# Kernel optimization log

Hardware: AMD Instinct MI355X
Metric: run time of the kernel (lower is better)

## Reference

```python
import jax, jax.numpy as jnp
import numpy as np

H, DH, HID = 8, 16, 128
N_USER, N_ITEM, N_TASTE, N_IMAGE = 20000, 50000, 50000, 50000


def setup_inputs() -> dict:
    key = jax.random.key(0)
    ks = jax.random.split(key, 24)
    f = jax.random.normal
    s = 1.0 / np.sqrt(HID).astype(np.float32)
    inp = {
        "x_user": f(ks[0], (N_USER, HID), jnp.float32),
        "x_item": f(ks[1], (N_ITEM, HID), jnp.float32),
        "x_taste": f(ks[2], (N_TASTE, HID), jnp.float32),
        "x_image": f(ks[3], (N_IMAGE, HID), jnp.float32),
        "Wk": f(ks[4], (4, HID, HID), jnp.float32) * s,
        "bk": jnp.zeros((4, HID), jnp.float32),
        "Wq": f(ks[5], (4, HID, HID), jnp.float32) * s,
        "bq": jnp.zeros((4, HID), jnp.float32),
        "Wv": f(ks[6], (4, HID, HID), jnp.float32) * s,
        "bv": jnp.zeros((4, HID), jnp.float32),
        "a_rel": f(ks[7], (4, H, DH, DH), jnp.float32) * (1.0 / np.sqrt(DH).astype(np.float32)),
        "m_rel": f(ks[8], (4, H, DH, DH), jnp.float32) * (1.0 / np.sqrt(DH).astype(np.float32)),
        "p_rel": jnp.ones((4, H), jnp.float32),
        "Wo": f(ks[9], (2, HID, HID), jnp.float32) * s,
        "bo": jnp.zeros((2, HID), jnp.float32),
        "skip": jnp.ones((2,), jnp.float32),
        "ti_src": jax.random.randint(ks[10], (50000,), 0, N_TASTE, jnp.int32),
        "ti_dst": jax.random.randint(ks[11], (50000,), 0, N_ITEM, jnp.int32),
        "im_src": jax.random.randint(ks[12], (50000,), 0, N_IMAGE, jnp.int32),
        "im_dst": jax.random.randint(ks[13], (50000,), 0, N_ITEM, jnp.int32),
        "ub_src": jax.random.randint(ks[14], (500000,), 0, N_USER, jnp.int32),
        "ub_dst": jax.random.randint(ks[15], (500000,), 0, N_ITEM, jnp.int32),
        "bu_src": jax.random.randint(ks[16], (500000,), 0, N_ITEM, jnp.int32),
        "bu_dst": jax.random.randint(ks[17], (500000,), 0, N_USER, jnp.int32),
    }
    return inp


def _kqv(x, i, Wk, bk, Wq, bq, Wv, bv):
    k = (x @ Wk[i] + bk[i]).reshape(-1, H, DH)
    q = (x @ Wq[i] + bq[i]).reshape(-1, H, DH)
    v = (x @ Wv[i] + bv[i]).reshape(-1, H, DH)
    return k, q, v


def _edge_alpha_msg(k_src, v_src, q_dst, src, dst, a, m, p):
    # per-edge-type relation transform at node level, then gather per edge
    kr = jnp.einsum('nhd,hde->nhe', k_src, a)  # [Nsrc,H,DH]
    vr = jnp.einsum('nhd,hde->nhe', v_src, m)
    alpha = (q_dst[dst] * kr[src]).sum(-1) * p * (1.0 / np.sqrt(DH).astype(np.float32))  # [E,H]
    return alpha, vr[src]


def _seg_softmax_agg(alpha, msg, dst, n):
    amax = jax.ops.segment_max(alpha, dst, num_segments=n)
    amax = jnp.where(jnp.isfinite(amax), amax, 0.0)
    ex = jnp.exp(alpha - amax[dst])
    den = jax.ops.segment_sum(ex, dst, num_segments=n)
    w = ex / (den[dst] + 1e-16)
    return jax.ops.segment_sum(msg * w[..., None], dst, num_segments=n)  # [n,H,DH]


def reference(x_user, x_item, x_taste, x_image, Wk, bk, Wq, bq, Wv, bv,
              a_rel, m_rel, p_rel, Wo, bo, skip,
              ti_src, ti_dst, im_src, im_dst, ub_src, ub_dst, bu_src, bu_dst):
    k_u, q_u, v_u = _kqv(x_user, 0, Wk, bk, Wq, bq, Wv, bv)
    k_i, q_i, v_i = _kqv(x_item, 1, Wk, bk, Wq, bq, Wv, bv)
    k_t, _, v_t = _kqv(x_taste, 2, Wk, bk, Wq, bq, Wv, bv)
    k_g, _, v_g = _kqv(x_image, 3, Wk, bk, Wq, bq, Wv, bv)

    # edges into 'item': taste(0), image(1), user-buys(2); softmax over all combined per item
    a0, m0 = _edge_alpha_msg(k_t, v_t, q_i, ti_src, ti_dst, a_rel[0], m_rel[0], p_rel[0])
    a1, m1 = _edge_alpha_msg(k_g, v_g, q_i, im_src, im_dst, a_rel[1], m_rel[1], p_rel[1])
    a2, m2 = _edge_alpha_msg(k_u, v_u, q_i, ub_src, ub_dst, a_rel[2], m_rel[2], p_rel[2])
    alpha_i = jnp.concatenate([a0, a1, a2], 0)
    msg_i = jnp.concatenate([m0, m1, m2], 0)
    dst_i = jnp.concatenate([ti_dst, im_dst, ub_dst], 0)
    agg_i = _seg_softmax_agg(alpha_i, msg_i, dst_i, N_ITEM)

    # edges into 'user': item-bought_by(3)
    a3, m3 = _edge_alpha_msg(k_i, v_i, q_u, bu_src, bu_dst, a_rel[3], m_rel[3], p_rel[3])
    agg_u = _seg_softmax_agg(a3, m3, bu_dst, N_USER)

    out_i = jax.nn.gelu(agg_i.reshape(-1, HID), approximate=False) @ Wo[0] + bo[0]
    g_i = jax.nn.sigmoid(skip[0])
    out_i = g_i * out_i + (1.0 - g_i) * x_item

    out_u = jax.nn.gelu(agg_u.reshape(-1, HID), approximate=False) @ Wo[1] + bo[1]
    g_u = jax.nn.sigmoid(skip[1])
    out_u = g_u * out_u + (1.0 - g_u) * x_user
    return (out_i, out_u)
```

## Files before the change

kernel.cpp:

```cpp
#include <hip/hip_runtime.h>
#include <math.h>


namespace {
constexpr int HIDN  = 128;
constexpr int NHEAD = 8;

constexpr int NU = 20000, NI = 50000, NT = 50000, NG = 50000;
constexpr int E_TI = 50000, E_IM = 50000, E_UB = 500000, E_BU = 500000;
constexpr int ETOT = E_TI + E_IM + E_UB + E_BU;
constexpr int ND   = NI + NU;

constexpr int BASE_U = 0;
constexpr int BASE_I = NU;
constexpr int BASE_T = NU + NI;
constexpr int BASE_G = NU + NI + NT;

constexpr int NMAT = 12;
constexpr int MATSZ = 128 * 128;
constexpr int SU = 136;

constexpr int NBU = (NU + 63) / 64;
constexpr int NBI = (NI + 63) / 64;
constexpr int NBT = (NT + 63) / 64;
constexpr int NBG = (NG + 63) / 64;
}

typedef __attribute__((ext_vector_type(8))) short short8v;
typedef __attribute__((ext_vector_type(4))) float f32x4;
typedef __attribute__((ext_vector_type(4))) unsigned short ushort4v;

__device__ __forceinline__ unsigned short bf16rne(float f) {
    unsigned u = __float_as_uint(f);
    unsigned r = (u + 0x7fffu + ((u >> 16) & 1u)) >> 16;
    return (unsigned short)r;
}
__device__ __forceinline__ float bf16f(unsigned short h) {
    return __uint_as_float(((unsigned)h) << 16);
}
__device__ __forceinline__ float bflo(unsigned int u) { return __uint_as_float(u << 16); }
__device__ __forceinline__ float bfhi(unsigned int u) { return __uint_as_float(u & 0xffff0000u); }

__global__ void build_cw_kernel(const float* __restrict__ Wk, const float* __restrict__ bk,
                                const float* __restrict__ Wv, const float* __restrict__ bv,
                                const float* __restrict__ a_rel, const float* __restrict__ m_rel,
                                float* __restrict__ cw)
{
    const int total = 2 * 4 * 129 * 128;
    int idx = blockIdx.x * blockDim.x + threadIdx.x;
    if (idx >= total) return;
    int c     = idx & 127;
    int r     = (idx >> 7) % 129;
    int t     = ((idx >> 7) / 129) & 3;
    int which = idx / (4 * 129 * 128);
    const int et_map[4] = {2, 3, 0, 1};
    int et = et_map[t];
    const float* W = (which == 0 ? Wk : Wv) + (size_t)t * HIDN * HIDN;
    const float* b = (which == 0 ? bk : bv) + (size_t)t * HIDN;
    const float* A = (which == 0 ? a_rel : m_rel) + (size_t)et * NHEAD * 16 * 16;
    int h = c >> 4, e2 = c & 15;
    float s = 0.f;
#pragma unroll
    for (int d = 0; d < 16; ++d) {
        float w = (r == 128) ? b[h * 16 + d] : W[(size_t)r * HIDN + h * 16 + d];
        s = fmaf(w, A[h * 256 + d * 16 + e2], s);
    }
    cw[idx] = s;
}

__global__ void pack_kernel(const float* __restrict__ cw,
                            const float* __restrict__ Wq, const float* __restrict__ bq,
                            const float* __restrict__ Wo, const float* __restrict__ bo,
                            short* __restrict__ pkh, short* __restrict__ pkl,
                            float* __restrict__ bias)
{
    const int total = NMAT * MATSZ + NMAT * HIDN;
    int idx = blockIdx.x * blockDim.x + threadIdx.x;
    if (idx >= total) return;
    if (idx < NMAT * MATSZ) {
        int mat = idx >> 14;
        int rem = idx & (MATSZ - 1);
        int i    = rem & 7;
        int lane = (rem >> 3) & 63;
        int ct   = (rem >> 9) & 7;
        int ks   = rem >> 12;
        int k   = ks * 32 + ((lane >> 4) & 3) * 8 + i;
        int col = ct * 16 + (lane & 15);
        float v;
        if (mat < 8)       v = cw[(size_t)mat * 129 * 128 + (size_t)k * 128 + col];
        else if (mat < 10) v = Wq[(size_t)(mat - 8) * MATSZ + (size_t)k * 128 + col];
        else               v = Wo[(size_t)(mat - 10) * MATSZ + (size_t)k * 128 + col];
        unsigned short hb = bf16rne(v);
        float rest = v - bf16f(hb);
        pkh[idx] = (short)hb;
        pkl[idx] = (short)bf16rne(rest);
    } else {
        int b = idx - NMAT * MATSZ;
        int mat = b >> 7, col = b & 127;
        float v;
        if (mat < 8)       v = cw[(size_t)mat * 129 * 128 + (size_t)128 * 128 + col];
        else if (mat < 10) v = bq[(mat - 8) * HIDN + col];
        else               v = bo[(mat - 10) * HIDN + col];
        bias[b] = v;
    }
}

__global__ __launch_bounds__(256) void mfma_proj_all(
    const float* __restrict__ xu, const float* __restrict__ xi,
    const float* __restrict__ xt, const float* __restrict__ xg,
    const short* __restrict__ pkh, const short* __restrict__ pkl,
    const float* __restrict__ bias,
    unsigned short* __restrict__ krb, unsigned short* __restrict__ vrb,
    unsigned short* __restrict__ qb_u, unsigned short* __restrict__ qb_i)
{
    int b = blockIdx.x;
    int seg, bloc;
    if (b < NBU)                  { seg = 0; bloc = b; }
    else if (b < NBU + NBI)       { seg = 1; bloc = b - NBU; }
    else if (b < NBU + NBI + NBT) { seg = 2; bloc = b - NBU - NBI; }
    else                          { seg = 3; bloc = b - NBU - NBI - NBT; }
    const float* x = (seg == 0) ? xu : (seg == 1) ? xi : (seg == 2) ? xt : xg;
    const int M     = (seg == 0) ? NU : (seg == 1) ? NI : (seg == 2) ? NT : NG;
    const int rbase = (seg == 0) ? BASE_U : (seg == 1) ? BASE_I : (seg == 2) ? BASE_T : BASE_G;
    unsigned short* qp = (seg == 0) ? qb_u : (seg == 1) ? qb_i : nullptr;

    __shared__ unsigned short hs[64 * SU];
    __shared__ unsigned short ls[64 * SU];
    const int t  = threadIdx.x;
    const int r0 = bloc * 64;
    const int rows = min(64, M - r0);

#pragma unroll
    for (int p = 0; p < 8; ++p) {
        int f = p * 256 + t;
        int row = f >> 5, c4 = f & 31;
        float4 v = make_float4(0.f, 0.f, 0.f, 0.f);
        if (row < rows) v = *(const float4*)(x + (size_t)(r0 + row) * HIDN + c4 * 4);
        float vv[4] = {v.x, v.y, v.z, v.w};
        ushort4v hq, lq;
#pragma unroll
        for (int i = 0; i < 4; ++i) {
            unsigned short hb = bf16rne(vv[i]);
            hq[i] = hb;
            lq[i] = bf16rne(vv[i] - bf16f(hb));
        }
        *(ushort4v*)&hs[row * SU + c4 * 4] = hq;
        *(ushort4v*)&ls[row * SU + c4 * 4] = lq;
    }
    __syncthreads();

    const int l = t & 63, w = t >> 6;
    const int kgrp = l >> 4;
    const int ct0  = 2 * w;
    const int ccol = l & 15;

    for (int mi = 0; mi < 3; ++mi) {
        if (mi == 2 && qp == nullptr) break;
        const int mat = (mi == 0) ? seg : (mi == 1) ? (4 + seg) : (8 + seg);
        const short8v* bh = (const short8v*)(pkh + (size_t)mat * MATSZ);
        const short8v* bl = (const short8v*)(pkl + (size_t)mat * MATSZ);
        const float*   bs = bias + mat * HIDN;

        short8v B1[4][2], B2[4][2];
#pragma unroll
        for (int ks = 0; ks < 4; ++ks) {
#pragma unroll
            for (int c = 0; c < 2; ++c) {
                B1[ks][c] = bh[(ks * 8 + ct0 + c) * 64 + l];
                if (mi == 2) B2[ks][c] = bl[(ks * 8 + ct0 + c) * 64 + l];
            }
        }

        const float bv0 = bs[(ct0 + 0) * 16 + ccol];
        const float bv1 = bs[(ct0 + 1) * 16 + ccol];

        for (int rt = 0; rt < 4; ++rt) {
            f32x4 a0, a1;
            a0[0]=0.f;a0[1]=0.f;a0[2]=0.f;a0[3]=0.f;
            a1[0]=0.f;a1[1]=0.f;a1[2]=0.f;a1[3]=0.f;
            const int arow = rt * 16 + ccol;
#pragma unroll
            for (int ks = 0; ks < 4; ++ks) {
                short8v ah = *(const short8v*)&hs[arow * SU + ks * 32 + kgrp * 8];
                short8v al = *(const short8v*)&ls[arow * SU + ks * 32 + kgrp * 8];
                a0 = __builtin_amdgcn_mfma_f32_16x16x32_bf16(ah, B1[ks][0], a0, 0, 0, 0);
                a1 = __builtin_amdgcn_mfma_f32_16x16x32_bf16(ah, B1[ks][1], a1, 0, 0, 0);
                a0 = __builtin_amdgcn_mfma_f32_16x16x32_bf16(al, B1[ks][0], a0, 0, 0, 0);
                a1 = __builtin_amdgcn_mfma_f32_16x16x32_bf16(al, B1[ks][1], a1, 0, 0, 0);
                if (mi == 2) {
                    a0 = __builtin_amdgcn_mfma_f32_16x16x32_bf16(ah, B2[ks][0], a0, 0, 0, 0);
                    a1 = __builtin_amdgcn_mfma_f32_16x16x32_bf16(ah, B2[ks][1], a1, 0, 0, 0);
                }
            }
            const int crow = r0 + rt * 16 + kgrp * 4;
            unsigned short* dst = (mi == 0) ? krb + (size_t)rbase * HIDN
                                : (mi == 1) ? vrb + (size_t)rbase * HIDN
                                            : qp;
#pragma unroll
            for (int j = 0; j < 4; ++j) {
                int grow = crow + j;
                if (grow < M) {
                    size_t o = (size_t)grow * HIDN;
                    dst[o + (ct0 + 0) * 16 + ccol] = bf16rne(a0[j] + bv0);
                    dst[o + (ct0 + 1) * 16 + ccol] = bf16rne(a1[j] + bv1);
                }
            }
        }
    }
}

__global__ __launch_bounds__(256) void mfma_out_all(
    const float* __restrict__ agg_i, const float* __restrict__ agg_u,
    const short* __restrict__ pkh, const short* __restrict__ pkl,
    const float* __restrict__ bias,
    const float* __restrict__ x_item, const float* __restrict__ x_user,
    const float* __restrict__ skip_ptr,
    float* __restrict__ outp)
{
    int b = blockIdx.x;
    int seg = (b < NBI) ? 0 : 1;
    int bloc = (seg == 0) ? b : b - NBI;
    const float* agg = (seg == 0) ? agg_i : agg_u;
    const float* xin = (seg == 0) ? x_item : x_user;
    const int M = (seg == 0) ? NI : NU;
    const int mat = 10 + seg;
    float* out = (seg == 0) ? outp : outp + (size_t)NI * HIDN;

    __shared__ unsigned short hs[64 * SU];
    __shared__ unsigned short ls[64 * SU];
    const int t  = threadIdx.x;
    const int r0 = bloc * 64;
    const int rows = min(64, M - r0);

#pragma unroll
    for (int p = 0; p < 8; ++p) {
        int f = p * 256 + t;
        int row = f >> 5, c4 = f & 31;
        float4 v = make_float4(0.f, 0.f, 0.f, 0.f);
        if (row < rows) v = *(const float4*)(agg + (size_t)(r0 + row) * HIDN + c4 * 4);
        float vv[4] = {v.x, v.y, v.z, v.w};
        ushort4v hq, lq;
#pragma unroll
        for (int i = 0; i < 4; ++i) {
            float g = 0.5f * vv[i] * (1.0f + erff(vv[i] * 0.70710678118654752440f));
            unsigned short hb = bf16rne(g);
            hq[i] = hb;
            lq[i] = bf16rne(g - bf16f(hb));
        }
        *(ushort4v*)&hs[row * SU + c4 * 4] = hq;
        *(ushort4v*)&ls[row * SU + c4 * 4] = lq;
    }
    __syncthreads();

    const int l = t & 63, w = t >> 6;
    const int kgrp = l >> 4;
    const int ct0  = 2 * w;
    const int ccol = l & 15;

    const short8v* bh = (const short8v*)(pkh + (size_t)mat * MATSZ);
    const short8v* bl = (const short8v*)(pkl + (size_t)mat * MATSZ);
    const float*   bs = bias + mat * HIDN;

    short8v B1[4][2], B2[4][2];
#pragma unroll
    for (int ks = 0; ks < 4; ++ks) {
#pragma unroll
        for (int c = 0; c < 2; ++c) {
            B1[ks][c] = bh[(ks * 8 + ct0 + c) * 64 + l];
            B2[ks][c] = bl[(ks * 8 + ct0 + c) * 64 + l];
        }
    }

    const float gate = 1.f / (1.f + expf(-skip_ptr[seg]));
    const float og = 1.f - gate;
    const float bv0 = bs[(ct0 + 0) * 16 + ccol];
    const float bv1 = bs[(ct0 + 1) * 16 + ccol];

    for (int rt = 0; rt < 4; ++rt) {
        f32x4 a0, a1;
        a0[0]=0.f;a0[1]=0.f;a0[2]=0.f;a0[3]=0.f;
        a1[0]=0.f;a1[1]=0.f;a1[2]=0.f;a1[3]=0.f;
        const int arow = rt * 16 + ccol;
#pragma unroll
        for (int ks = 0; ks < 4; ++ks) {
            short8v ah = *(const short8v*)&hs[arow * SU + ks * 32 + kgrp * 8];
            short8v al = *(const short8v*)&ls[arow * SU + ks * 32 + kgrp * 8];
            a0 = __builtin_amdgcn_mfma_f32_16x16x32_bf16(ah, B1[ks][0], a0, 0, 0, 0);
            a1 = __builtin_amdgcn_mfma_f32_16x16x32_bf16(ah, B1[ks][1], a1, 0, 0, 0);
            a0 = __builtin_amdgcn_mfma_f32_16x16x32_bf16(al, B1[ks][0], a0, 0, 0, 0);
            a1 = __builtin_amdgcn_mfma_f32_16x16x32_bf16(al, B1[ks][1], a1, 0, 0, 0);
            a0 = __builtin_amdgcn_mfma_f32_16x16x32_bf16(ah, B2[ks][0], a0, 0, 0, 0);
            a1 = __builtin_amdgcn_mfma_f32_16x16x32_bf16(ah, B2[ks][1], a1, 0, 0, 0);
        }
        const int crow = r0 + rt * 16 + kgrp * 4;
#pragma unroll
        for (int j = 0; j < 4; ++j) {
            int grow = crow + j;
            if (grow < M) {
                size_t o = (size_t)grow * HIDN;
                size_t o0 = o + (ct0 + 0) * 16 + ccol;
                size_t o1 = o + (ct0 + 1) * 16 + ccol;
                out[o0] = gate * (a0[j] + bv0) + og * xin[o0];
                out[o1] = gate * (a1[j] + bv1) + og * xin[o1];
            }
        }
    }
}


__global__ void hist_kernel(const int* __restrict__ ti_dst, const int* __restrict__ im_dst,
                            const int* __restrict__ ub_dst, const int* __restrict__ bu_dst,
                            int* __restrict__ deg)
{
    int i = blockIdx.x * blockDim.x + threadIdx.x;
    if (i >= ETOT) return;
    int d;
    if (i < E_TI)                     d = ti_dst[i];
    else if (i < E_TI + E_IM)         d = im_dst[i - E_TI];
    else if (i < E_TI + E_IM + E_UB)  d = ub_dst[i - E_TI - E_IM];
    else                              d = NI + bu_dst[i - E_TI - E_IM - E_UB];
    atomicAdd(&deg[d], 1);
}

__global__ void scan1_kernel(int* __restrict__ deg, int* __restrict__ tops, int n)
{
    __shared__ int sh[256];
    int i = blockIdx.x * 256 + threadIdx.x;
    int v = (i < n) ? deg[i] : 0;
    sh[threadIdx.x] = v;
    __syncthreads();
    for (int o = 1; o < 256; o <<= 1) {
        int t = (threadIdx.x >= o) ? sh[threadIdx.x - o] : 0;
        __syncthreads();
        sh[threadIdx.x] += t;
        __syncthreads();
    }
    if (i < n) deg[i] = sh[threadIdx.x];
    if (threadIdx.x == 255) tops[blockIdx.x] = sh[255];
}

__global__ void scan2_kernel(int* __restrict__ tops, int nb)
{
    __shared__ int sh[1024];
    int v = (threadIdx.x < nb) ? tops[threadIdx.x] : 0;
    sh[threadIdx.x] = v;
    __syncthreads();
    for (int o = 1; o < 1024; o <<= 1) {
        int t = (threadIdx.x >= o) ? sh[threadIdx.x - o] : 0;
        __syncthreads();
        sh[threadIdx.x] += t;
        __syncthreads();
    }
    if (threadIdx.x < nb) tops[threadIdx.x] = sh[threadIdx.x];
}

__global__ void scan3_kernel(const int* __restrict__ part, const int* __restrict__ tops,
                             int* __restrict__ rowptr, int* __restrict__ cursor, int n)
{
    int i = blockIdx.x * 256 + threadIdx.x;
    if (i >= n) return;
    int add = (blockIdx.x > 0) ? tops[blockIdx.x - 1] : 0;
    int prev = (i > 0) ? ((threadIdx.x > 0) ? part[i - 1] + add
                                            : ((blockIdx.x > 0) ? tops[blockIdx.x - 1] : 0))
                       : 0;
    rowptr[i + 1] = part[i] + add;
    cursor[i] = prev;
    if (i == 0) rowptr[0] = 0;
}

__global__ void scatter_kernel(const int* __restrict__ ti_src, const int* __restrict__ ti_dst,
                               const int* __restrict__ im_src, const int* __restrict__ im_dst,
                               const int* __restrict__ ub_src, const int* __restrict__ ub_dst,
                               const int* __restrict__ bu_src, const int* __restrict__ bu_dst,
                               int* __restrict__ cursor, int* __restrict__ col)
{
    int i = blockIdx.x * blockDim.x + threadIdx.x;
    if (i >= ETOT) return;
    int d, row, et;
    if (i < E_TI)                    { d = ti_dst[i];                 row = BASE_T + ti_src[i];                 et = 0; }
    else if (i < E_TI + E_IM)        { int e = i - E_TI;              row = BASE_G + im_src[e]; d = im_dst[e];  et = 1; }
    else if (i < E_TI + E_IM + E_UB) { int e = i - E_TI - E_IM;       row = BASE_U + ub_src[e]; d = ub_dst[e];  et = 2; }
    else                             { int e = i - E_TI - E_IM - E_UB; row = BASE_I + bu_src[e]; d = NI + bu_dst[e]; et = 3; }
    int p = atomicAdd(&cursor[d], 1);
    col[p] = (row << 2) | et;
}

__global__ __launch_bounds__(256) void f12_kernel(
    const int* __restrict__ rowptr, const int* __restrict__ rowend,
    const int* __restrict__ col,
    const unsigned int* __restrict__ krw,
    const unsigned int* __restrict__ qb_i, const unsigned int* __restrict__ qb_u,
    const unsigned int* __restrict__ vrw,
    const float* __restrict__ prel,
    float* __restrict__ agg_i, float* __restrict__ agg_u)
{
    int wid = (blockIdx.x << 2) + (threadIdx.x >> 6);
    if (wid >= ND) return;
    const int l = threadIdx.x & 63;
    const int h = l >> 3;

    unsigned int qu = (wid < NI) ? qb_i[(size_t)wid * 64 + l]
                                 : qb_u[(size_t)(wid - NI) * 64 + l];
    float2 qv = make_float2(bflo(qu), bfhi(qu));
    const float pr0 = prel[h]      * 0.25f;
    const float pr1 = prel[8 + h]  * 0.25f;
    const float pr2 = prel[16 + h] * 0.25f;
    const float pr3 = prel[24 + h] * 0.25f;

    const int start = rowptr[wid], end = rowend[wid];
    float m = -3.0e38f, ax = 0.f, ay = 0.f, den = 0.f;

    int p = start;
    for (; p + 1 < end; p += 2) {
        int pk0 = col[p], pk1 = col[p + 1];
        unsigned int u0 = krw[(size_t)(pk0 >> 2) * 64 + l];
        unsigned int u1 = krw[(size_t)(pk1 >> 2) * 64 + l];
        unsigned int v0 = vrw[(size_t)(pk0 >> 2) * 64 + l];
        unsigned int v1 = vrw[(size_t)(pk1 >> 2) * 64 + l];
        float d0 = qv.x * bflo(u0) + qv.y * bfhi(u0);
        float d1 = qv.x * bflo(u1) + qv.y * bfhi(u1);
        d0 += __shfl_xor(d0, 1); d1 += __shfl_xor(d1, 1);
        d0 += __shfl_xor(d0, 2); d1 += __shfl_xor(d1, 2);
        d0 += __shfl_xor(d0, 4); d1 += __shfl_xor(d1, 4);
        int e0t = pk0 & 3, e1t = pk1 & 3;
        float f0 = (e0t & 2) ? ((e0t & 1) ? pr3 : pr2) : ((e0t & 1) ? pr1 : pr0);
        float f1 = (e1t & 2) ? ((e1t & 1) ? pr3 : pr2) : ((e1t & 1) ? pr1 : pr0);
        float a0 = d0 * f0;
        float a1 = d1 * f1;
        float mn = fmaxf(m, fmaxf(a0, a1));
        float s  = __expf(m - mn);
        float e0 = __expf(a0 - mn);
        float e1 = __expf(a1 - mn);
        ax = ax * s + e0 * bflo(v0) + e1 * bflo(v1);
        ay = ay * s + e0 * bfhi(v0) + e1 * bfhi(v1);
        den = den * s + e0 + e1;
        m = mn;
    }
    if (p < end) {
        int pk0 = col[p];
        unsigned int u0 = krw[(size_t)(pk0 >> 2) * 64 + l];
        unsigned int v0 = vrw[(size_t)(pk0 >> 2) * 64 + l];
        float d0 = qv.x * bflo(u0) + qv.y * bfhi(u0);
        d0 += __shfl_xor(d0, 1);
        d0 += __shfl_xor(d0, 2);
        d0 += __shfl_xor(d0, 4);
        int e0t = pk0 & 3;
        float f0 = (e0t & 2) ? ((e0t & 1) ? pr3 : pr2) : ((e0t & 1) ? pr1 : pr0);
        float a0 = d0 * f0;
        float mn = fmaxf(m, a0);
        float s  = __expf(m - mn);
        float e0 = __expf(a0 - mn);
        ax = ax * s + e0 * bflo(v0);
        ay = ay * s + e0 * bfhi(v0);
        den = den * s + e0;
    }

    float inv = 1.f / (den + 1e-16f);
    float* dst = (wid < NI) ? agg_i + (size_t)wid * HIDN
                            : agg_u + (size_t)(wid - NI) * HIDN;
    *(float2*)(dst + 2 * l) = make_float2(ax * inv, ay * inv);
}

extern "C" void kernel_launch(void* const* d_in, const int* in_sizes, int n_in,
                              void* d_out, int out_size, void* d_ws, size_t ws_size,
                              hipStream_t stream)
{
    const float* x_user = (const float*)d_in[0];
    const float* x_item = (const float*)d_in[1];
    const float* x_taste= (const float*)d_in[2];
    const float* x_image= (const float*)d_in[3];
    const float* Wk     = (const float*)d_in[4];
    const float* bk     = (const float*)d_in[5];
    const float* Wq     = (const float*)d_in[6];
    const float* bq     = (const float*)d_in[7];
    const float* Wv     = (const float*)d_in[8];
    const float* bv     = (const float*)d_in[9];
    const float* a_rel  = (const float*)d_in[10];
    const float* m_rel  = (const float*)d_in[11];
    const float* p_rel  = (const float*)d_in[12];
    const float* Wo     = (const float*)d_in[13];
    const float* bo     = (const float*)d_in[14];
    const float* skip   = (const float*)d_in[15];
    const int* ti_src = (const int*)d_in[16];
    const int* ti_dst = (const int*)d_in[17];
    const int* im_src = (const int*)d_in[18];
    const int* im_dst = (const int*)d_in[19];
    const int* ub_src = (const int*)d_in[20];
    const int* ub_dst = (const int*)d_in[21];
    const int* bu_src = (const int*)d_in[22];
    const int* bu_dst = (const int*)d_in[23];

    float* ws = (float*)d_ws;
    float* outp = (float*)d_out;
    (void)in_sizes; (void)n_in; (void)out_size;

    size_t off = 0;
    auto alloc = [&](size_t n) { size_t o = off; off += n; return o; };
    const size_t o_cw   = alloc((size_t)2 * 4 * 129 * 128);
    const size_t o_pkh  = alloc((size_t)NMAT * MATSZ / 2);
    const size_t o_pkl  = alloc((size_t)NMAT * MATSZ / 2);
    const size_t o_bias = alloc((size_t)NMAT * HIDN);
    const size_t o_krb  = alloc((size_t)(NU + NI + NT + NG) * HIDN / 2);
    const size_t o_vrb  = alloc((size_t)(NU + NI + NT + NG) * HIDN / 2);
    const size_t o_q_i  = alloc((size_t)NI * HIDN / 2);
    const size_t o_q_u  = alloc((size_t)NU * HIDN / 2);
    const size_t o_agg  = alloc((size_t)(NI + NU) * HIDN);
    const size_t o_int  = alloc((size_t)(ND + 1) + ND + 1024 + ETOT);

    if (ws_size < off * sizeof(float)) return;

    unsigned short* krb  = (unsigned short*)(ws + o_krb);
    unsigned short* vrb  = (unsigned short*)(ws + o_vrb);
    unsigned short* qb_i = (unsigned short*)(ws + o_q_i);
    unsigned short* qb_u = (unsigned short*)(ws + o_q_u);

    short* pkh  = (short*)(ws + o_pkh);
    short* pkl  = (short*)(ws + o_pkl);
    float* bias = ws + o_bias;

    int* deg    = (int*)(ws + o_cw);
    int* rowptr = (int*)(ws + o_int);
    int* cursor = rowptr + (ND + 1);
    int* tops   = cursor + ND;
    int* col    = tops + 1024;

    float* agg_i = ws + o_agg;
    float* agg_u = ws + o_agg + (size_t)NI * HIDN;

    {
        int total = 2 * 4 * 129 * 128;
        build_cw_kernel<<<(total + 255) / 256, 256, 0, stream>>>(
            Wk, bk, Wv, bv, a_rel, m_rel, ws + o_cw);
        int ptotal = NMAT * MATSZ + NMAT * HIDN;
        pack_kernel<<<(ptotal + 255) / 256, 256, 0, stream>>>(
            ws + o_cw, Wq, bq, Wo, bo, pkh, pkl, bias);
    }

    mfma_proj_all<<<NBU + NBI + NBT + NBG, 256, 0, stream>>>(
        x_user, x_item, x_taste, x_image, pkh, pkl, bias,
        krb, vrb, qb_u, qb_i);

    hipMemsetAsync(deg, 0, ND * sizeof(int), stream);
    hist_kernel<<<(ETOT + 255) / 256, 256, 0, stream>>>(ti_dst, im_dst, ub_dst, bu_dst, deg);
    const int NB1 = (ND + 255) / 256;
    scan1_kernel<<<NB1, 256, 0, stream>>>(deg, tops, ND);
    scan2_kernel<<<1, 1024, 0, stream>>>(tops, NB1);
    scan3_kernel<<<NB1, 256, 0, stream>>>(deg, tops, rowptr, cursor, ND);
    scatter_kernel<<<(ETOT + 255) / 256, 256, 0, stream>>>(
        ti_src, ti_dst, im_src, im_dst, ub_src, ub_dst, bu_src, bu_dst, cursor, col);

    const int NBW = (ND + 3) / 4;
    f12_kernel<<<NBW, 256, 0, stream>>>(
        rowptr, cursor, col,
        (const unsigned int*)krb, (const unsigned int*)qb_i, (const unsigned int*)qb_u,
        (const unsigned int*)vrb, p_rel,
        agg_i, agg_u);

    mfma_out_all<<<NBI + NBU, 256, 0, stream>>>(
        agg_i, agg_u, pkh, pkl, bias, x_item, x_user, skip, outp);
}
```

Before: 337.4 us.

## Fold p_rel scaling into composed key weights and unroll edge loop by four

The per-head relation prior p_rel/sqrt(DH) is folded into the precomputed key-relation weight matrix and bias, so the edge kernel no longer needs an edge type tag or a per-edge scale select. Column entries become plain row indices. The online-softmax edge loop is unrolled from two to four edges per iteration, which puts more independent gathers in flight. This costs more registers per lane and adds a bf16 rounding of the scaled keys.

Result: faster. 328.4 us (-2.7%).

```diff
diff --git a/kernel.cpp b/kernel.cpp
--- a/kernel.cpp
+++ b/kernel.cpp
@@ -44,6 +44,7 @@
 __global__ void build_cw_kernel(const float* __restrict__ Wk, const float* __restrict__ bk,
                                 const float* __restrict__ Wv, const float* __restrict__ bv,
                                 const float* __restrict__ a_rel, const float* __restrict__ m_rel,
+                                const float* __restrict__ p_rel,
                                 float* __restrict__ cw)
 {
     const int total = 2 * 4 * 129 * 128;
@@ -65,6 +66,7 @@
         float w = (r == 128) ? b[h * 16 + d] : W[(size_t)r * HIDN + h * 16 + d];
         s = fmaf(w, A[h * 256 + d * 16 + e2], s);
     }
+    if (which == 0) s *= p_rel[et * NHEAD + h] * 0.25f;
     cw[idx] = s;
 }
 
@@ -376,13 +378,13 @@
 {
     int i = blockIdx.x * blockDim.x + threadIdx.x;
     if (i >= ETOT) return;
-    int d, row, et;
-    if (i < E_TI)                    { d = ti_dst[i];                 row = BASE_T + ti_src[i];                 et = 0; }
-    else if (i < E_TI + E_IM)        { int e = i - E_TI;              row = BASE_G + im_src[e]; d = im_dst[e];  et = 1; }
-    else if (i < E_TI + E_IM + E_UB) { int e = i - E_TI - E_IM;       row = BASE_U + ub_src[e]; d = ub_dst[e];  et = 2; }
-    else                             { int e = i - E_TI - E_IM - E_UB; row = BASE_I + bu_src[e]; d = NI + bu_dst[e]; et = 3; }
+    int d, row;
+    if (i < E_TI)                    { d = ti_dst[i];                  row = BASE_T + ti_src[i]; }
+    else if (i < E_TI + E_IM)        { int e = i - E_TI;               row = BASE_G + im_src[e]; d = im_dst[e]; }
+    else if (i < E_TI + E_IM + E_UB) { int e = i - E_TI - E_IM;        row = BASE_U + ub_src[e]; d = ub_dst[e]; }
+    else                             { int e = i - E_TI - E_IM - E_UB; row = BASE_I + bu_src[e]; d = NI + bu_dst[e]; }
     int p = atomicAdd(&cursor[d], 1);
-    col[p] = (row << 2) | et;
+    col[p] = row;
 }
 
 __global__ __launch_bounds__(256) void f12_kernel(
@@ -391,68 +393,66 @@
     const unsigned int* __restrict__ krw,
     const unsigned int* __restrict__ qb_i, const unsigned int* __restrict__ qb_u,
     const unsigned int* __restrict__ vrw,
-    const float* __restrict__ prel,
     float* __restrict__ agg_i, float* __restrict__ agg_u)
 {
     int wid = (blockIdx.x << 2) + (threadIdx.x >> 6);
     if (wid >= ND) return;
     const int l = threadIdx.x & 63;
-    const int h = l >> 3;
 
     unsigned int qu = (wid < NI) ? qb_i[(size_t)wid * 64 + l]
                                  : qb_u[(size_t)(wid - NI) * 64 + l];
-    float2 qv = make_float2(bflo(qu), bfhi(qu));
-    const float pr0 = prel[h]      * 0.25f;
-    const float pr1 = prel[8 + h]  * 0.25f;
-    const float pr2 = prel[16 + h] * 0.25f;
-    const float pr3 = prel[24 + h] * 0.25f;
+    const float qx = bflo(qu), qy = bfhi(qu);
 
     const int start = rowptr[wid], end = rowend[wid];
     float m = -3.0e38f, ax = 0.f, ay = 0.f, den = 0.f;
 
     int p = start;
-    for (; p + 1 < end; p += 2) {
-        int pk0 = col[p], pk1 = col[p + 1];
-        unsigned int u0 = krw[(size_t)(pk0 >> 2) * 64 + l];
-        unsigned int u1 = krw[(size_t)(pk1 >> 2) * 64 + l];
-        unsigned int v0 = vrw[(size_t)(pk0 >> 2) * 64 + l];
-        unsigned int v1 = vrw[(size_t)(pk1 >> 2) * 64 + l];
-        float d0 = qv.x * bflo(u0) + qv.y * bfhi(u0);
-        float d1 = qv.x * bflo(u1) + qv.y * bfhi(u1);
+    for (; p + 3 < end; p += 4) {
+        int r0_ = col[p], r1_ = col[p + 1], r2_ = col[p + 2], r3_ = col[p + 3];
+        unsigned int u0 = krw[(size_t)r0_ * 64 + l];
+        unsigned int u1 = krw[(size_t)r1_ * 64 + l];
+        unsigned int u2 = krw[(size_t)r2_ * 64 + l];
+        unsigned int u3 = krw[(size_t)r3_ * 64 + l];
+        unsigned int v0 = vrw[(size_t)r0_ * 64 + l];
+        unsigned int v1 = vrw[(size_t)r1_ * 64 + l];
+        unsigned int v2 = vrw[(size_t)r2_ * 64 + l];
+        unsigned int v3 = vrw[(size_t)r3_ * 64 + l];
+        float d0 = qx * bflo(u0) + qy * bfhi(u0);
+        float d1 = qx * bflo(u1) + qy * bfhi(u1);
+        float d2 = qx * bflo(u2) + qy * bfhi(u2);
+        float d3 = qx * bflo(u3) + qy * bfhi(u3);
         d0 += __shfl_xor(d0, 1); d1 += __shfl_xor(d1, 1);
+        d2 += __shfl_xor(d2, 1); d3 += __shfl_xor(d3, 1);
         d0 += __shfl_xor(d0, 2); d1 += __shfl_xor(d1, 2);
+        d2 += __shfl_xor(d2, 2); d3 += __shfl_xor(d3, 2);
         d0 += __shfl_xor(d0, 4); d1 += __shfl_xor(d1, 4);
-        int e0t = pk0 & 3, e1t = pk1 & 3;
-        float f0 = (e0t & 2) ? ((e0t & 1) ? pr3 : pr2) : ((e0t & 1) ? pr1 : pr0);
-        float f1 = (e1t & 2) ? ((e1t & 1) ? pr3 : pr2) : ((e1t & 1) ? pr1 : pr0);
-        float a0 = d0 * f0;
-        float a1 = d1 * f1;
-        float mn = fmaxf(m, fmaxf(a0, a1));
+        d2 += __shfl_xor(d2, 4); d3 += __shfl_xor(d3, 4);
+        float mn = fmaxf(m, fmaxf(fmaxf(d0, d1), fmaxf(d2, d3)));
         float s  = __expf(m - mn);
-        float e0 = __expf(a0 - mn);
-        float e1 = __expf(a1 - mn);
-        ax = ax * s + e0 * bflo(v0) + e1 * bflo(v1);
-        ay = ay * s + e0 * bfhi(v0) + e1 * bfhi(v1);
-        den = den * s + e0 + e1;
+        float e0 = __expf(d0 - mn);
+        float e1 = __expf(d1 - mn);
+        float e2 = __expf(d2 - mn);
+        float e3 = __expf(d3 - mn);
+        ax = ax * s + e0 * bflo(v0) + e1 * bflo(v1) + e2 * bflo(v2) + e3 * bflo(v3);
+        ay = ay * s + e0 * bfhi(v0) + e1 * bfhi(v1) + e2 * bfhi(v2) + e3 * bfhi(v3);
+        den = den * s + (e0 + e1) + (e2 + e3);
         m = mn;
     }
-    if (p < end) {
-        int pk0 = col[p];
-        unsigned int u0 = krw[(size_t)(pk0 >> 2) * 64 + l];
-        unsigned int v0 = vrw[(size_t)(pk0 >> 2) * 64 + l];
-        float d0 = qv.x * bflo(u0) + qv.y * bfhi(u0);
+    for (; p < end; ++p) {
+        int r0_ = col[p];
+        unsigned int u0 = krw[(size_t)r0_ * 64 + l];
+        unsigned int v0 = vrw[(size_t)r0_ * 64 + l];
+        float d0 = qx * bflo(u0) + qy * bfhi(u0);
         d0 += __shfl_xor(d0, 1);
         d0 += __shfl_xor(d0, 2);
         d0 += __shfl_xor(d0, 4);
-        int e0t = pk0 & 3;
-        float f0 = (e0t & 2) ? ((e0t & 1) ? pr3 : pr2) : ((e0t & 1) ? pr1 : pr0);
-        float a0 = d0 * f0;
-        float mn = fmaxf(m, a0);
+        float mn = fmaxf(m, d0);
         float s  = __expf(m - mn);
-        float e0 = __expf(a0 - mn);
+        float e0 = __expf(d0 - mn);
         ax = ax * s + e0 * bflo(v0);
         ay = ay * s + e0 * bfhi(v0);
         den = den * s + e0;
+        m = mn;
     }
 
     float inv = 1.f / (den + 1e-16f);
@@ -530,7 +530,7 @@
     {
         int total = 2 * 4 * 129 * 128;
         build_cw_kernel<<<(total + 255) / 256, 256, 0, stream>>>(
-            Wk, bk, Wv, bv, a_rel, m_rel, ws + o_cw);
+            Wk, bk, Wv, bv, a_rel, m_rel, p_rel, ws + o_cw);
         int ptotal = NMAT * MATSZ + NMAT * HIDN;
         pack_kernel<<<(ptotal + 255) / 256, 256, 0, stream>>>(
             ws + o_cw, Wq, bq, Wo, bo, pkh, pkl, bias);
@@ -553,7 +553,7 @@
     f12_kernel<<<NBW, 256, 0, stream>>>(
         rowptr, cursor, col,
         (const unsigned int*)krb, (const unsigned int*)qb_i, (const unsigned int*)qb_u,
-        (const unsigned int*)vrb, p_rel,
+        (const unsigned int*)vrb,
         agg_i, agg_u);
 
     mfma_out_all<<<NBI + NBU, 256, 0, stream>>>(
```
